# Kernel optimization log

Hardware: AMD Instinct MI355X
Metric: run time of the kernel (lower is better)

Reference implementation:

```python
import jax, jax.numpy as jnp
import numpy as np

N_NODES = 100000
N_EDGES = 1600000
IN_FEAT = 48
OUT_FEAT = 48


def setup_inputs() -> dict:
    key = jax.random.key(0)
    k_h, k_src, k_dst, k_tw, k_tb, k_pw, k_pb = jax.random.split(key, 7)
    lim = 1.0 / np.sqrt(IN_FEAT)  # nn.Linear default init range
    return {
        "h": jax.random.normal(k_h, (N_NODES, IN_FEAT), dtype=jnp.float32),
        "theta_w": jax.random.uniform(k_tw, (OUT_FEAT, IN_FEAT), jnp.float32, -lim, lim),
        "theta_b": jax.random.uniform(k_tb, (OUT_FEAT,), jnp.float32, -lim, lim),
        "phi_w": jax.random.uniform(k_pw, (OUT_FEAT, IN_FEAT), jnp.float32, -lim, lim),
        "phi_b": jax.random.uniform(k_pb, (OUT_FEAT,), jnp.float32, -lim, lim),
        "src": jax.random.randint(k_src, (N_EDGES,), 0, N_NODES, dtype=jnp.int64),
        "dst": jax.random.randint(k_dst, (N_EDGES,), 0, N_NODES, dtype=jnp.int64),
    }


def reference(h, theta_w, theta_b, phi_w, phi_b, src, dst):
    # phi is applied to source node features only -> compute per-node then gather (cheaper, same math)
    phi_all = h @ phi_w.T + phi_b                      # [N, Dout]
    diff = h[dst] - h[src]                             # [E, Din]  (edges.dst['x'] - edges.src['x'])
    e = diff @ theta_w.T + theta_b + phi_all[src]      # [E, Dout] per-edge message
    # scatter-max over incoming edges per destination node
    out = jax.ops.segment_max(e, dst, num_segments=N_NODES)  # [N, Dout]
    # nodes with no in-edges: DGL yields 0, segment_max yields -inf -> replace
    out = jnp.where(jnp.isneginf(out), 0.0, out)
    return out
```

## Files before the change

kernel.cpp:

```cpp
#include <hip/hip_runtime.h>
#include <math.h>

#define DIN 48
#define DOUT 48
#define NPB 64
#define NB_MAX 1600
#define BIN_BLOCKS 512
#define EPB_MAX 3136
#define NPART 8
#define PCAP 256
#define SCAP 1344
#define KSTR 49
#define BSTR 64
#define INIT_KEY 0x007FFFFFu
#define NTB_THREADS 512

typedef short s16x8 __attribute__((ext_vector_type(8)));
typedef float f32x4v __attribute__((ext_vector_type(4)));

__device__ __forceinline__ float funkey(unsigned k) {
  unsigned b = (k & 0x80000000u) ? (k & 0x7FFFFFFFu) : ~k;
  return __uint_as_float(b);
}
__device__ __forceinline__ unsigned bfkey(unsigned u16) {
  unsigned b = u16 << 16;
  return (b & 0x80000000u) ? ~b : (b | 0x80000000u);
}
__device__ __forceinline__ unsigned short f2bf(float f) {
  unsigned u = __float_as_uint(f);
  return (unsigned short)((u + 0x7fffu + ((u >> 16) & 1u)) >> 16);
}

__global__ __launch_bounds__(256) void prep(
    const float* __restrict__ tw, const float* __restrict__ tb,
    const float* __restrict__ pw, const float* __restrict__ pb,
    unsigned short* __restrict__ wcs, float* __restrict__ bias,
    unsigned* __restrict__ gcnt, int ngcnt) {
  int i = blockIdx.x * 256 + threadIdx.x;
  if (i < 6144) {
    int j = i & 7;
    int fragpos = i >> 3;
    int lane = fragpos & 63;
    int frag = fragpos >> 6;
    int kstep = frag & 1;
    int ntile = frag >> 1;
    int feat = ntile * 16 + (lane & 15);
    int k = kstep * 32 + (lane >> 4) * 8 + j;
    float v = 0.f;
    if (k < DIN) {
      v = (feat < DOUT) ? tw[feat * DIN + k]
                        : pw[(feat - DOUT) * DIN + k] - tw[(feat - DOUT) * DIN + k];
    }
    wcs[i] = f2bf(v);
  } else if (i < 6144 + 96) {
    int f = i - 6144;
    bias[f] = (f < DOUT) ? tb[f] : pb[f - DOUT];
  } else if (i >= 6240 && i < 6240 + ngcnt) {
    gcnt[i - 6240] = 0u;
  }
}

__device__ __forceinline__ void transform_body(
    int bid, const float* __restrict__ h, const unsigned short* __restrict__ wcs,
    const float* __restrict__ bias, float* __restrict__ A,
    unsigned short* __restrict__ Bh, int n_nodes) {
  int t = threadIdx.x;
  int wave = t >> 6, lane = t & 63;
  int quad = lane >> 4, nl = lane & 15;
  int vb = bid * 128 + wave * 16;
  int vload = vb + nl;

  s16x8 a0 = {0, 0, 0, 0, 0, 0, 0, 0};
  s16x8 a1 = {0, 0, 0, 0, 0, 0, 0, 0};
  if (vload < n_nodes) {
    const float* hp = h + (size_t)vload * DIN;
    float4 x = *reinterpret_cast<const float4*>(hp + quad * 8);
    float4 y = *reinterpret_cast<const float4*>(hp + quad * 8 + 4);
    a0[0] = (short)f2bf(x.x); a0[1] = (short)f2bf(x.y);
    a0[2] = (short)f2bf(x.z); a0[3] = (short)f2bf(x.w);
    a0[4] = (short)f2bf(y.x); a0[5] = (short)f2bf(y.y);
    a0[6] = (short)f2bf(y.z); a0[7] = (short)f2bf(y.w);
    if (quad < 2) {
      float4 z = *reinterpret_cast<const float4*>(hp + 32 + quad * 8);
      float4 u = *reinterpret_cast<const float4*>(hp + 32 + quad * 8 + 4);
      a1[0] = (short)f2bf(z.x); a1[1] = (short)f2bf(z.y);
      a1[2] = (short)f2bf(z.z); a1[3] = (short)f2bf(z.w);
      a1[4] = (short)f2bf(u.x); a1[5] = (short)f2bf(u.y);
      a1[6] = (short)f2bf(u.z); a1[7] = (short)f2bf(u.w);
    }
  }

  const s16x8* wf = reinterpret_cast<const s16x8*>(wcs);
  f32x4v acc[6];
#pragma unroll
  for (int nt = 0; nt < 6; ++nt) {
    float bv = bias[nt * 16 + nl];
    acc[nt] = (f32x4v){bv, bv, bv, bv};
  }
#pragma unroll
  for (int nt = 0; nt < 6; ++nt) {
    s16x8 b0 = wf[(nt * 2 + 0) * 64 + lane];
    s16x8 b1 = wf[(nt * 2 + 1) * 64 + lane];
    acc[nt] = __builtin_amdgcn_mfma_f32_16x16x32_bf16(a0, b0, acc[nt], 0, 0, 0);
    acc[nt] = __builtin_amdgcn_mfma_f32_16x16x32_bf16(a1, b1, acc[nt], 0, 0, 0);
  }

#pragma unroll
  for (int reg = 0; reg < 4; ++reg) {
    int v = vb + quad * 4 + reg;
    if (v < n_nodes) {
#pragma unroll
      for (int nt = 0; nt < 3; ++nt)
        A[(size_t)v * DOUT + nt * 16 + nl] = acc[nt][reg];
#pragma unroll
      for (int nt = 3; nt < 6; ++nt)
        Bh[(size_t)v * BSTR + (nt - 3) * 16 + nl] = f2bf(acc[nt][reg]);
    }
  }
}

__device__ __forceinline__ void bin_body(
    int r, unsigned* __restrict__ shmem,
    const int* __restrict__ src, const int* __restrict__ dst,
    unsigned* __restrict__ ebuf, unsigned* __restrict__ gcnt,
    int n_edges, int nbucket, int epb) {
  unsigned* rec = shmem;
  unsigned short* rbkt = (unsigned short*)(rec + EPB_MAX);
  unsigned* cnt = (unsigned*)(rbkt + EPB_MAX);
  int t = threadIdx.x;
  int pid = r & (NPART - 1);
  unsigned* gc = gcnt + (size_t)pid * nbucket;
  unsigned* eb = ebuf + (size_t)pid * nbucket * PCAP;

  for (int b = t; b < nbucket; b += NTB_THREADS) cnt[b] = 0;
  __syncthreads();

  int start = r * epb;
  int nrec = n_edges - start;
  if (nrec > epb) nrec = epb;
  if (nrec < 0) nrec = 0;

  for (int k = t; k < nrec; k += NTB_THREADS) {
    int s = src[start + k], d = dst[start + k];
    int b = d >> 6;
    rec[k] = ((unsigned)(d & (NPB - 1)) << 17) | (unsigned)s;
    rbkt[k] = (unsigned short)b;
    atomicAdd(&cnt[b], 1u);
  }
  __syncthreads();

  for (int b = t; b < nbucket; b += NTB_THREADS) {
    unsigned c = cnt[b];
    if (c) cnt[b] = atomicAdd(&gc[b], c);
  }
  __syncthreads();

  for (int k = t; k < nrec; k += NTB_THREADS) {
    unsigned b = rbkt[k];
    unsigned p = atomicAdd(&cnt[b], 1u);
    if (p < (unsigned)PCAP) eb[(size_t)b * PCAP + p] = rec[k];
  }
}

__global__ __launch_bounds__(NTB_THREADS) void nt_bin(
    const float* __restrict__ h, const unsigned short* __restrict__ wcs,
    const float* __restrict__ bias, float* __restrict__ A,
    unsigned short* __restrict__ Bh, const int* __restrict__ src,
    const int* __restrict__ dst, unsigned* __restrict__ ebuf,
    unsigned* __restrict__ gcnt, int n_nodes, int n_edges, int nbucket,
    int epb) {
  __shared__ unsigned shmem[EPB_MAX + EPB_MAX / 2 + NB_MAX];
  int bid = blockIdx.x;
  if (bid < BIN_BLOCKS)
    bin_body(bid, shmem, src, dst, ebuf, gcnt, n_edges, nbucket, epb);
  else
    transform_body(bid - BIN_BLOCKS, h, wcs, bias, A, Bh, n_nodes);
}

#define BM_THREADS 256
#define BM_GROUPS 21
#define PFD 8
__global__ __launch_bounds__(BM_THREADS) void bucket_max(
    const unsigned* __restrict__ ebuf, const unsigned* __restrict__ gcnt,
    const unsigned short* __restrict__ Bh, float* __restrict__ out,
    int n_nodes, int nbucket) {
  __shared__ unsigned keys[NPB * KSTR];
  __shared__ unsigned srecs[SCAP];
  int t = threadIdx.x;
  int bkt = blockIdx.x;

#pragma unroll
  for (int i = t; i < NPB * KSTR; i += BM_THREADS) keys[i] = INIT_KEY;

  unsigned off = 0;
#pragma unroll
  for (int p = 0; p < NPART; ++p) {
    unsigned tp = gcnt[(size_t)p * nbucket + bkt];
    if (tp > (unsigned)PCAP) tp = PCAP;
    if (off + tp > (unsigned)SCAP) tp = SCAP - off;
    const unsigned* ep = ebuf + ((size_t)p * nbucket + bkt) * PCAP;
    for (unsigned i = t; i < tp; i += BM_THREADS) srecs[off + i] = ep[i];
    off += tp;
  }
  __syncthreads();
  int tot = (int)off;

  int g = t / 12;
  int c = t % 12;
  if (g < BM_GROUPS) {
    int lo = g * tot / BM_GROUPS;
    int hi = (g + 1) * tot / BM_GROUPS;
    for (int j = lo; j < hi; j += PFD) {
      int n = hi - j;
      if (n > PFD) n = PFD;
      unsigned rr[PFD];
      uint2 bb[PFD];
#pragma unroll
      for (int p = 0; p < PFD; ++p)
        if (p < n) rr[p] = srecs[j + p];
#pragma unroll
      for (int p = 0; p < PFD; ++p)
        if (p < n)
          bb[p] = *reinterpret_cast<const uint2*>(
              Bh + (size_t)(rr[p] & 0x1FFFF) * BSTR + c * 4);
#pragma unroll
      for (int p = 0; p < PFD; ++p) {
        if (p < n) {
          unsigned* kp = &keys[(rr[p] >> 17) * KSTR + c];
          atomicMax(&kp[0],  bfkey(bb[p].x & 0xffffu));
          atomicMax(&kp[12], bfkey(bb[p].x >> 16));
          atomicMax(&kp[24], bfkey(bb[p].y & 0xffffu));
          atomicMax(&kp[36], bfkey(bb[p].y >> 16));
        }
      }
    }
  }
  __syncthreads();

  int node0 = bkt * NPB;
  for (int i = t; i < NPB * (DOUT / 4); i += BM_THREADS) {
    int n = i / (DOUT / 4), cc = i % (DOUT / 4);
    int v = node0 + n;
    if (v < n_nodes) {
      unsigned* kp = &keys[n * KSTR + cc];
      unsigned k0 = kp[0], k1 = kp[12], k2 = kp[24], k3 = kp[36];
      float4* op = reinterpret_cast<float4*>(out + (size_t)v * DOUT + 4 * cc);
      float4 aa = *op;
      float4 r;
      r.x = (k0 == INIT_KEY) ? 0.f : aa.x + funkey(k0);
      r.y = (k1 == INIT_KEY) ? 0.f : aa.y + funkey(k1);
      r.z = (k2 == INIT_KEY) ? 0.f : aa.z + funkey(k2);
      r.w = (k3 == INIT_KEY) ? 0.f : aa.w + funkey(k3);
      *op = r;
    }
  }
}

extern "C" void kernel_launch(void* const* d_in, const int* in_sizes, int n_in,
                              void* d_out, int out_size, void* d_ws, size_t ws_size,
                              hipStream_t stream) {
  const float* h  = (const float*)d_in[0];
  const float* tw = (const float*)d_in[1];
  const float* tb = (const float*)d_in[2];
  const float* pw = (const float*)d_in[3];
  const float* pb = (const float*)d_in[4];
  const int* src  = (const int*)d_in[5];
  const int* dst  = (const int*)d_in[6];
  int n_nodes = in_sizes[0] / DIN;
  int n_edges = in_sizes[5];
  int nbucket = (n_nodes + NPB - 1) / NPB;
  int epb = (n_edges + BIN_BLOCKS - 1) / BIN_BLOCKS;
  int ngcnt = NPART * nbucket;

  unsigned short* Bh  = (unsigned short*)d_ws;
  unsigned* ebuf      = (unsigned*)(Bh + (size_t)n_nodes * BSTR);
  unsigned* gcnt      = ebuf + (size_t)NPART * nbucket * PCAP;
  unsigned short* wcs = (unsigned short*)(gcnt + ngcnt);
  float* bias         = (float*)(wcs + 6144);
  float* A            = (float*)d_out;

  int nt_blocks = (n_nodes + 127) / 128;

  prep<<<74, 256, 0, stream>>>(tw, tb, pw, pb, wcs, bias, gcnt, ngcnt);
  nt_bin<<<BIN_BLOCKS + nt_blocks, NTB_THREADS, 0, stream>>>(
      h, wcs, bias, A, Bh, src, dst, ebuf, gcnt, n_nodes, n_edges, nbucket,
      epb);
  bucket_max<<<nbucket, BM_THREADS, 0, stream>>>(ebuf, gcnt, Bh, A, n_nodes,
                                                 nbucket);
}
```

Before: 144.5 us.

## Counting-sort bucket edges by node and reduce max in registers

Replaces per-feature shared-memory atomicMax into a keys table with a per-block counting sort of edge records by destination node, then each 12-lane group walks a contiguous node range, keeping running maxima in registers and writing each node's result once. Groups are split at node boundaries so no two groups share a node. This removes the LDS atomics and the keys-table initialization. In exchange it adds a histogram, a scan and a scatter pass with shared atomics, plus possible load imbalance across groups, and zero-degree nodes are zeroed in a separate pass.

Measured after the change: 158.5 us. +9.7%, slower.

```diff
diff --git a/kernel.cpp b/kernel.cpp
--- a/kernel.cpp
+++ b/kernel.cpp
@@ -10,7 +10,6 @@
 #define NPART 8
 #define PCAP 256
 #define SCAP 1344
-#define KSTR 49
 #define BSTR 64
 #define INIT_KEY 0x007FFFFFu
 #define NTB_THREADS 512
@@ -178,19 +177,21 @@
 }
 
 #define BM_THREADS 256
-#define BM_GROUPS 21
+#define NGROUP 20
 #define PFD 8
 __global__ __launch_bounds__(BM_THREADS) void bucket_max(
     const unsigned* __restrict__ ebuf, const unsigned* __restrict__ gcnt,
     const unsigned short* __restrict__ Bh, float* __restrict__ out,
     int n_nodes, int nbucket) {
-  __shared__ unsigned keys[NPB * KSTR];
   __shared__ unsigned srecs[SCAP];
+  __shared__ unsigned sorted[SCAP];
+  __shared__ unsigned cnt64[NPB];
+  __shared__ unsigned nstart[NPB];
+  __shared__ unsigned npos[NPB];
   int t = threadIdx.x;
   int bkt = blockIdx.x;
 
-#pragma unroll
-  for (int i = t; i < NPB * KSTR; i += BM_THREADS) keys[i] = INIT_KEY;
+  if (t < NPB) cnt64[t] = 0;
 
   unsigned off = 0;
 #pragma unroll
@@ -205,53 +206,123 @@
   __syncthreads();
   int tot = (int)off;
 
-  int g = t / 12;
-  int c = t % 12;
-  if (g < BM_GROUPS) {
-    int lo = g * tot / BM_GROUPS;
-    int hi = (g + 1) * tot / BM_GROUPS;
-    for (int j = lo; j < hi; j += PFD) {
-      int n = hi - j;
-      if (n > PFD) n = PFD;
-      unsigned rr[PFD];
-      uint2 bb[PFD];
-#pragma unroll
-      for (int p = 0; p < PFD; ++p)
-        if (p < n) rr[p] = srecs[j + p];
-#pragma unroll
-      for (int p = 0; p < PFD; ++p)
-        if (p < n)
+  for (int i = t; i < tot; i += BM_THREADS)
+    atomicAdd(&cnt64[srecs[i] >> 17], 1u);
+  __syncthreads();
+
+  if (t < NPB) {
+    unsigned v = cnt64[t];
+    unsigned s = v;
+#pragma unroll
+    for (int o = 1; o < NPB; o <<= 1) {
+      unsigned u = __shfl_up(s, o, 64);
+      if (t >= o) s += u;
+    }
+    nstart[t] = s - v;
+    npos[t] = s - v;
+  }
+  __syncthreads();
+
+  for (int i = t; i < tot; i += BM_THREADS) {
+    unsigned r = srecs[i];
+    unsigned p = atomicAdd(&npos[r >> 17], 1u);
+    sorted[p] = r;
+  }
+  __syncthreads();
+
+  int wave = t >> 6, lane = t & 63;
+  int gil = lane / 12;
+  int c = lane % 12;
+  int g = wave * 5 + gil;
+  int node0 = bkt * NPB;
+
+  if (gil < 5 && tot > 0) {
+    unsigned lo_e = (unsigned)tot, hi_e = (unsigned)tot;
+    bool fl = false, fh = false;
+#pragma unroll 8
+    for (int n = 0; n < NPB; ++n) {
+      unsigned st = nstart[n];
+      unsigned gn = (unsigned)(((unsigned long long)st * NGROUP) / (unsigned)tot);
+      if (!fl && gn >= (unsigned)g)       { lo_e = st; fl = true; }
+      if (!fh && gn >= (unsigned)(g + 1)) { hi_e = st; fh = true; break; }
+    }
+    if (!fl) lo_e = hi_e;
+
+    if (lo_e < hi_e) {
+      unsigned m0 = INIT_KEY, m1 = INIT_KEY, m2 = INIT_KEY, m3 = INIT_KEY;
+      unsigned cur = sorted[lo_e] >> 17;
+      unsigned j = lo_e;
+      for (; j + PFD <= hi_e; j += PFD) {
+        unsigned rr[PFD];
+        uint2 bb[PFD];
+#pragma unroll
+        for (int p = 0; p < PFD; ++p) rr[p] = sorted[j + p];
+#pragma unroll
+        for (int p = 0; p < PFD; ++p)
           bb[p] = *reinterpret_cast<const uint2*>(
               Bh + (size_t)(rr[p] & 0x1FFFF) * BSTR + c * 4);
 #pragma unroll
-      for (int p = 0; p < PFD; ++p) {
-        if (p < n) {
-          unsigned* kp = &keys[(rr[p] >> 17) * KSTR + c];
-          atomicMax(&kp[0],  bfkey(bb[p].x & 0xffffu));
-          atomicMax(&kp[12], bfkey(bb[p].x >> 16));
-          atomicMax(&kp[24], bfkey(bb[p].y & 0xffffu));
-          atomicMax(&kp[36], bfkey(bb[p].y >> 16));
+        for (int p = 0; p < PFD; ++p) {
+          unsigned n = rr[p] >> 17;
+          if (n != cur) {
+            int v = node0 + (int)cur;
+            if (v < n_nodes) {
+              float4* op = reinterpret_cast<float4*>(out + (size_t)v * DOUT + c * 4);
+              float4 aa = *op;
+              aa.x += funkey(m0); aa.y += funkey(m1);
+              aa.z += funkey(m2); aa.w += funkey(m3);
+              *op = aa;
+            }
+            m0 = m1 = m2 = m3 = INIT_KEY;
+            cur = n;
+          }
+          m0 = max(m0, bfkey(bb[p].x & 0xffffu));
+          m1 = max(m1, bfkey(bb[p].x >> 16));
+          m2 = max(m2, bfkey(bb[p].y & 0xffffu));
+          m3 = max(m3, bfkey(bb[p].y >> 16));
         }
       }
-    }
-  }
-  __syncthreads();
-
-  int node0 = bkt * NPB;
-  for (int i = t; i < NPB * (DOUT / 4); i += BM_THREADS) {
-    int n = i / (DOUT / 4), cc = i % (DOUT / 4);
+      for (; j < hi_e; ++j) {
+        unsigned r0 = sorted[j];
+        unsigned n = r0 >> 17;
+        if (n != cur) {
+          int v = node0 + (int)cur;
+          if (v < n_nodes) {
+            float4* op = reinterpret_cast<float4*>(out + (size_t)v * DOUT + c * 4);
+            float4 aa = *op;
+            aa.x += funkey(m0); aa.y += funkey(m1);
+            aa.z += funkey(m2); aa.w += funkey(m3);
+            *op = aa;
+          }
+          m0 = m1 = m2 = m3 = INIT_KEY;
+          cur = n;
+        }
+        uint2 b0 = *reinterpret_cast<const uint2*>(
+            Bh + (size_t)(r0 & 0x1FFFF) * BSTR + c * 4);
+        m0 = max(m0, bfkey(b0.x & 0xffffu));
+        m1 = max(m1, bfkey(b0.x >> 16));
+        m2 = max(m2, bfkey(b0.y & 0xffffu));
+        m3 = max(m3, bfkey(b0.y >> 16));
+      }
+      {
+        int v = node0 + (int)cur;
+        if (v < n_nodes) {
+          float4* op = reinterpret_cast<float4*>(out + (size_t)v * DOUT + c * 4);
+          float4 aa = *op;
+          aa.x += funkey(m0); aa.y += funkey(m1);
+          aa.z += funkey(m2); aa.w += funkey(m3);
+          *op = aa;
+        }
+      }
+    }
+  }
+
+  for (int i = t; i < NPB * 12; i += BM_THREADS) {
+    int n = i / 12, cc = i % 12;
     int v = node0 + n;
-    if (v < n_nodes) {
-      unsigned* kp = &keys[n * KSTR + cc];
-      unsigned k0 = kp[0], k1 = kp[12], k2 = kp[24], k3 = kp[36];
-      float4* op = reinterpret_cast<float4*>(out + (size_t)v * DOUT + 4 * cc);
-      float4 aa = *op;
-      float4 r;
-      r.x = (k0 == INIT_KEY) ? 0.f : aa.x + funkey(k0);
-      r.y = (k1 == INIT_KEY) ? 0.f : aa.y + funkey(k1);
-      r.z = (k2 == INIT_KEY) ? 0.f : aa.z + funkey(k2);
-      r.w = (k3 == INIT_KEY) ? 0.f : aa.w + funkey(k3);
-      *op = r;
+    if (v < n_nodes && cnt64[n] == 0) {
+      float4 z = {0.f, 0.f, 0.f, 0.f};
+      *reinterpret_cast<float4*>(out + (size_t)v * DOUT + cc * 4) = z;
     }
   }
 }
```
